# Kernel optimization log

Hardware: AMD Instinct MI355X
Metric: run time of the kernel (lower is better)

The kernel has to match this reference:

```python
import jax, jax.numpy as jnp
import numpy as np


def setup_inputs() -> dict:
    key = jax.random.key(0)
    k1, k2, k3, k4 = jax.random.split(key, 4)
    B, S, E, H = 8, 2048, 1024, 64
    x = jax.random.normal(k1, (B, S, E), dtype=jnp.float32)
    scale = 1.0 / np.sqrt(E)
    Wq = jax.random.normal(k2, (E, H), dtype=jnp.float32) * scale
    Wk = jax.random.normal(k3, (E, H), dtype=jnp.float32) * scale
    Wv = jax.random.normal(k4, (E, H), dtype=jnp.float32) * scale
    return {"x": x, "Wq": Wq, "Wk": Wk, "Wv": Wv}


def reference(x, Wq, Wk, Wv):
    # x: [B, S, E]; Wq/Wk/Wv: [E, H]
    B, S, E = x.shape
    H = Wq.shape[1]
    q = x @ Wq  # [B, S, H]
    k = x @ Wk
    v = x @ Wv
    inv_sqrt_h = 1.0 / jnp.sqrt(jnp.asarray(H, dtype=x.dtype))
    att = jnp.einsum("bqh,bkh->bqk", q, k) * inv_sqrt_h  # [B, S, S]
    causal = jnp.tril(jnp.ones((S, S), dtype=bool))
    att = jnp.where(causal, att, jnp.asarray(-jnp.inf, dtype=att.dtype))
    att = jax.nn.softmax(att, axis=-1)
    # dropout p=0.0 (eval) -> identity
    return jnp.einsum("bqk,bkh->bqh", att, v)  # [B, S, H]
```

## Files before the change

kernel.cpp:

```cpp
#include <hip/hip_runtime.h>
#include <math.h>

typedef __attribute__((ext_vector_type(8))) short bf16x8;
typedef __attribute__((ext_vector_type(16))) float fx16;

#define SEQ 2048
#define HD 64

__device__ __forceinline__ unsigned f2bf_bits(float f){
  unsigned u = __float_as_uint(f);
  return (u + 0x7fffu + ((u >> 16) & 1u)) >> 16;
}
__device__ __forceinline__ unsigned cvt_pk_bf16(float a, float b){
  unsigned r;
  asm("v_cvt_pk_bf16_f32 %0, %1, %2" : "=v"(r) : "v"(a), "v"(b));
  return r;
}
union U8 { bf16x8 v; short s[8]; unsigned u[4]; };

__device__ __forceinline__ fx16 mfma_bf16(bf16x8 a, bf16x8 b, fx16 c){
  return __builtin_amdgcn_mfma_f32_32x32x16_bf16(a, b, c, 0, 0, 0);
}
__device__ __forceinline__ fx16 fzero(){
  fx16 z;
#pragma unroll
  for (int i = 0; i < 16; ++i) z[i] = 0.f;
  return z;
}

__global__ __launch_bounds__(256) void wconv_kernel(
    const float* __restrict__ Wq, const float* __restrict__ Wk, const float* __restrict__ Wv,
    short* __restrict__ wsB)
{
  int gid = blockIdx.x * 4 + (threadIdx.x >> 6);
  int lane = threadIdx.x & 63;
  int l31 = lane & 31, h = lane >> 5;
  int half = gid & 1;
  int rem = gid >> 1;
  int t = rem % 6;
  int stage = rem / 6;
  int n = t * 32 + l31;
  int mat = n >> 6, col = n & 63;
  const float* W = (mat == 0) ? Wq : (mat == 1) ? Wk : Wv;
  int kbase = stage * 16 + h * 8;
  U8 o;
#pragma unroll
  for (int i = 0; i < 8; ++i) {
    float f = W[(size_t)(kbase + i) * 64 + col];
    unsigned hb = f2bf_bits(f);
    if (half == 0) o.s[i] = (short)hb;
    else {
      float hf = __uint_as_float(hb << 16);
      o.s[i] = (short)f2bf_bits(f - hf);
    }
  }
  *(bf16x8*)(wsB + (size_t)gid * 512 + lane * 8) = o.v;
}

__global__ __launch_bounds__(256, 2) void proj_kernel(
    const float* __restrict__ x, const short* __restrict__ wsB,
    short* __restrict__ qh, short* __restrict__ ql,
    short* __restrict__ kh, short* __restrict__ kl,
    short* __restrict__ vth, short* __restrict__ vtl)
{
  __shared__ float Vb[64 * 68];

  const int tid = threadIdx.x;
  const int lane = tid & 63, w = tid >> 6;
  const int l31 = lane & 31, h = lane >> 5;
  const int m = w & 1;
  const int nset = (w >> 1) * 3;
  const int row0 = blockIdx.x * 64;
  const size_t xrow = (size_t)(row0 + m * 32 + l31) * 1024;

  fx16 accP[3], accQ[3];
#pragma unroll
  for (int t = 0; t < 3; ++t) { accP[t] = fzero(); accQ[t] = fzero(); }

  float4 A0[4][2], A1[4][2];
  bf16x8 B0[6], B1[6];

#define LOADA(AB, C1)                                                   \
  {                                                                     \
    _Pragma("unroll")                                                   \
    for (int ks = 0; ks < 4; ++ks) {                                    \
      int k = (C1) * 64 + ks * 16 + h * 8;                              \
      AB[ks][0] = *(const float4*)(x + xrow + k);                       \
      AB[ks][1] = *(const float4*)(x + xrow + k + 4);                   \
    }                                                                   \
  }

#define LOADB(BB, SR)                                                   \
  {                                                                     \
    _Pragma("unroll")                                                   \
    for (int tt = 0; tt < 3; ++tt) {                                    \
      size_t g2 = ((size_t)(SR) * 6 + nset + tt) * 2;                   \
      BB[tt * 2 + 0] = *(const bf16x8*)(wsB + g2 * 512 + lane * 8);     \
      BB[tt * 2 + 1] = *(const bf16x8*)(wsB + (g2 + 1) * 512 + lane * 8);\
    }                                                                   \
  }

#define STEP(AF, BB)                                                    \
  {                                                                     \
    U8 ah, al;                                                          \
    float xf[8];                                                        \
    xf[0] = AF[0].x; xf[1] = AF[0].y; xf[2] = AF[0].z; xf[3] = AF[0].w; \
    xf[4] = AF[1].x; xf[5] = AF[1].y; xf[6] = AF[1].z; xf[7] = AF[1].w; \
    _Pragma("unroll")                                                   \
    for (int i = 0; i < 8; ++i) {                                       \
      unsigned hb = f2bf_bits(xf[i]);                                   \
      ah.s[i] = (short)hb;                                              \
      float hf = __uint_as_float(hb << 16);                             \
      al.s[i] = (short)f2bf_bits(xf[i] - hf);                           \
    }                                                                   \
    _Pragma("unroll")                                                   \
    for (int tt = 0; tt < 3; ++tt) {                                    \
      accP[tt] = mfma_bf16(ah.v, BB[tt * 2 + 0], accP[tt]);             \
      accQ[tt] = mfma_bf16(ah.v, BB[tt * 2 + 1], accQ[tt]);             \
      accQ[tt] = mfma_bf16(al.v, BB[tt * 2 + 0], accQ[tt]);             \
    }                                                                   \
  }

#define CHUNK(C, ACUR, ANEXT)                                           \
  {                                                                     \
    if ((C) < 15) LOADA(ANEXT, (C) + 1);                                \
    STEP(ACUR[0], B0); if ((C) * 4 + 2 < 64) LOADB(B0, (C) * 4 + 2);    \
    STEP(ACUR[1], B1); if ((C) * 4 + 3 < 64) LOADB(B1, (C) * 4 + 3);    \
    STEP(ACUR[2], B0); if ((C) * 4 + 4 < 64) LOADB(B0, (C) * 4 + 4);    \
    STEP(ACUR[3], B1); if ((C) * 4 + 5 < 64) LOADB(B1, (C) * 4 + 5);    \
  }

  LOADA(A0, 0);
  LOADB(B0, 0);
  LOADB(B1, 1);
  for (int c2 = 0; c2 < 8; ++c2) {
    CHUNK(2 * c2 + 0, A0, A1);
    CHUNK(2 * c2 + 1, A1, A0);
  }
#undef CHUNK
#undef STEP
#undef LOADB
#undef LOADA

#pragma unroll
  for (int t = 0; t < 3; ++t) {
    int nt = nset + t;
    int mat = nt >> 1;
    int colb = (nt & 1) * 32 + l31;
    if (mat < 2) {
      short* dh = (mat == 0) ? qh : kh;
      short* dl = (mat == 0) ? ql : kl;
#pragma unroll
      for (int r = 0; r < 16; ++r) {
        float f = accP[t][r] + accQ[t][r];
        int rowg = row0 + m * 32 + (r & 3) + 8 * (r >> 2) + 4 * h;
        unsigned hb = f2bf_bits(f);
        float hf = __uint_as_float(hb << 16);
        unsigned lb = f2bf_bits(f - hf);
        dh[(size_t)rowg * 64 + colb] = (short)hb;
        dl[(size_t)rowg * 64 + colb] = (short)lb;
      }
    } else {
#pragma unroll
      for (int r = 0; r < 16; ++r) {
        float f = accP[t][r] + accQ[t][r];
        int srel = m * 32 + (r & 3) + 8 * (r >> 2) + 4 * h;
        Vb[srel * 68 + (nt - 4) * 32 + l31] = f;
      }
    }
  }
  __syncthreads();
  {
    int d = tid >> 2, sc = (tid & 3) * 16;
    int bb = row0 >> 11, s0 = row0 & 2047;
    U8 hv0, hv1, lv0, lv1;
#pragma unroll
    for (int ss = 0; ss < 16; ++ss) {
      float f = Vb[(sc + ss) * 68 + d];
      unsigned hb = f2bf_bits(f);
      float hf = __uint_as_float(hb << 16);
      unsigned lb = f2bf_bits(f - hf);
      if (ss < 8) { hv0.s[ss] = (short)hb; lv0.s[ss] = (short)lb; }
      else        { hv1.s[ss - 8] = (short)hb; lv1.s[ss - 8] = (short)lb; }
    }
    size_t o = (size_t)(bb * 64 + d) * 2048 + s0 + sc;
    *(bf16x8*)(vth + o) = hv0.v;  *(bf16x8*)(vth + o + 8) = hv1.v;
    *(bf16x8*)(vtl + o) = lv0.v;  *(bf16x8*)(vtl + o + 8) = lv1.v;
  }
}

__global__ __launch_bounds__(256, 2) void attn_kernel(
    const short* __restrict__ qh, const short* __restrict__ ql,
    const short* __restrict__ kh, const short* __restrict__ kl,
    const short* __restrict__ vth, const short* __restrict__ vtl,
    float* __restrict__ segO, float* __restrict__ segL, float* __restrict__ segM)
{
  __shared__ short Kbuf[2][64 * 128];
  __shared__ short Vbuf[2][64 * 128];

  const int bid = blockIdx.x;
  const int b = bid / 40;
  const int j = bid % 40;
  int qt, ch, nch;
  if (j < 4)       { nch = 1; qt = j;               ch = 0; }
  else if (j < 12) { nch = 2; qt = 4 + (j - 4) / 2; ch = (j - 4) % 2; }
  else if (j < 24) { nch = 3; qt = 8 + (j - 12) / 3; ch = (j - 12) % 3; }
  else             { nch = 4; qt = 12 + (j - 24) / 4; ch = (j - 24) % 4; }
  const int S = 2 * qt + 2;
  const int bs = S / nch, rem = S % nch;
  const int nsteps = bs + (ch < rem ? 1 : 0);
  const int kt0 = ch * bs + (ch < rem ? ch : rem);

  const int tid = threadIdx.x;
  const int lane = tid & 63, w = tid >> 6;
  const int l31 = lane & 31, h = lane >> 5;
  const int qabs = qt * 128 + w * 32 + l31;

  bf16x8 qf0[4], qf1[4];
  {
    size_t qrow = ((size_t)b * 2048 + qabs) * 64;
#pragma unroll
    for (int ds = 0; ds < 4; ++ds) {
      qf0[ds] = *(const bf16x8*)(qh + qrow + ds * 16 + 8 * h);
      qf1[ds] = *(const bf16x8*)(ql + qrow + ds * 16 + 8 * h);
    }
  }

  const int slot = tid & 15;
  const int half = slot >> 3;
  const int sb = (slot & 7) << 4;
  const int rbase = tid >> 4;
  const int d0 = (sb ^ ((rbase & 7) << 4)) >> 1;
  const short* ksrc = half ? kl : kh;
  const short* vsrc = half ? vtl : vth;
  const int woff = rbase * 256 + half * 128 + sb;

  fx16 accA0 = fzero(), accA1 = fzero(), accB0 = fzero(), accB1 = fzero();
  float Mrun = -3e38f, lrun = 0.f;
  const int sw = (l31 & 7) << 4;

  bf16x8 kreg[4], vreg[4];
#pragma unroll
  for (int jj = 0; jj < 4; ++jj) {
    kreg[jj] = *(const bf16x8*)(ksrc + ((size_t)b * 2048 + (size_t)kt0 * 64 + rbase + 16 * jj) * 64 + d0);
    vreg[jj] = *(const bf16x8*)(vsrc + ((size_t)(b * 64 + rbase + 16 * jj)) * 2048 + kt0 * 64 + d0);
  }
#pragma unroll
  for (int jj = 0; jj < 4; ++jj) {
    *(bf16x8*)((char*)Kbuf[0] + woff + jj * 4096) = kreg[jj];
    *(bf16x8*)((char*)Vbuf[0] + woff + jj * 4096) = vreg[jj];
  }
  __syncthreads();

  for (int it = 0; it < nsteps; ++it) {
    const int kt = kt0 + it;
    const int p = it & 1;
    const bool hasnext = (it + 1 < nsteps);
    if (hasnext) {
      int kn = kt + 1;
#pragma unroll
      for (int jj = 0; jj < 4; ++jj) {
        kreg[jj] = *(const bf16x8*)(ksrc + ((size_t)b * 2048 + (size_t)kn * 64 + rbase + 16 * jj) * 64 + d0);
        vreg[jj] = *(const bf16x8*)(vsrc + ((size_t)(b * 64 + rbase + 16 * jj)) * 2048 + kn * 64 + d0);
      }
    }

#pragma unroll
    for (int ms = 0; ms < 2; ++ms) {
      fx16 stA = fzero(), stB = fzero(), stC = fzero();
      {
        const char* arow = (const char*)Kbuf[p] + (ms * 32 + l31) * 256;
#pragma unroll
        for (int ds = 0; ds < 4; ++ds) {
          const int kb = ds * 32 + 16 * h;
          bf16x8 ah = *(const bf16x8*)(arow + (kb ^ sw));
          bf16x8 al = *(const bf16x8*)(arow + 128 + (kb ^ sw));
          stA = mfma_bf16(ah, qf0[ds], stA);
          stB = mfma_bf16(ah, qf1[ds], stB);
          stC = mfma_bf16(al, qf0[ds], stC);
        }
      }
      float sv[16];
      const int kbase = kt * 64 + ms * 32;
      const bool diag = (kbase + 31 > qt * 128 + w * 32);
#pragma unroll
      for (int r = 0; r < 16; ++r) {
        float s = (stA[r] + stB[r] + stC[r]) * 0.125f;
        if (diag) {
          int ka = kbase + (r & 3) + 8 * (r >> 2) + 4 * h;
          if (ka > qabs) s = -3e38f;
        }
        sv[r] = s;
      }
      float tm = sv[0];
#pragma unroll
      for (int r = 1; r < 16; ++r) tm = fmaxf(tm, sv[r]);
      tm = fmaxf(tm, __shfl_xor(tm, 32, 64));
      float Mnew = fmaxf(Mrun, tm);
      float alpha = __expf(Mrun - Mnew);
      Mrun = Mnew;
      float pvv[16]; float psum = 0.f;
#pragma unroll
      for (int r = 0; r < 16; ++r) { pvv[r] = __expf(sv[r] - Mnew); psum += pvv[r]; }
      psum += __shfl_xor(psum, 32, 64);
      lrun = lrun * alpha + psum;
#pragma unroll
      for (int r = 0; r < 16; ++r) {
        accA0[r] *= alpha; accA1[r] *= alpha; accB0[r] *= alpha; accB1[r] *= alpha;
      }
      unsigned chv[8], clv[8];
#pragma unroll
      for (int q2 = 0; q2 < 8; ++q2) {
        unsigned c = cvt_pk_bf16(pvv[2 * q2], pvv[2 * q2 + 1]);
        chv[q2] = c;
        float f0 = __uint_as_float(c << 16);
        float f1 = __uint_as_float(c & 0xffff0000u);
        clv[q2] = cvt_pk_bf16(pvv[2 * q2] - f0, pvv[2 * q2 + 1] - f1);
      }
#pragma unroll
      for (int kp = 0; kp < 2; ++kp) {
        U8 ph, pl;
        {
          unsigned c0 = chv[4 * kp], c1 = chv[4 * kp + 1], c2 = chv[4 * kp + 2], c3 = chv[4 * kp + 3];
          unsigned x0 = (unsigned)__shfl_xor((int)c0, 32, 64);
          unsigned x1 = (unsigned)__shfl_xor((int)c1, 32, 64);
          unsigned x2 = (unsigned)__shfl_xor((int)c2, 32, 64);
          unsigned x3 = (unsigned)__shfl_xor((int)c3, 32, 64);
          ph.u[0] = h ? x2 : c0;  ph.u[1] = h ? x3 : c1;
          ph.u[2] = h ? c2 : x0;  ph.u[3] = h ? c3 : x1;
          c0 = clv[4 * kp]; c1 = clv[4 * kp + 1]; c2 = clv[4 * kp + 2]; c3 = clv[4 * kp + 3];
          x0 = (unsigned)__shfl_xor((int)c0, 32, 64);
          x1 = (unsigned)__shfl_xor((int)c1, 32, 64);
          x2 = (unsigned)__shfl_xor((int)c2, 32, 64);
          x3 = (unsigned)__shfl_xor((int)c3, 32, 64);
          pl.u[0] = h ? x2 : c0;  pl.u[1] = h ? x3 : c1;
          pl.u[2] = h ? c2 : x0;  pl.u[3] = h ? c3 : x1;
        }
        const int kbv = ms * 64 + kp * 32 + 16 * h;
#pragma unroll
        for (int md = 0; md < 2; ++md) {
          const char* vrow = (const char*)Vbuf[p] + (md * 32 + l31) * 256;
          bf16x8 vh = *(const bf16x8*)(vrow + (kbv ^ sw));
          bf16x8 vl = *(const bf16x8*)(vrow + 128 + (kbv ^ sw));
          if (md == 0) {
            accA0 = mfma_bf16(vh, ph.v, accA0);
            accB0 = mfma_bf16(vh, pl.v, accB0);
            accB0 = mfma_bf16(vl, ph.v, accB0);
          } else {
            accA1 = mfma_bf16(vh, ph.v, accA1);
            accB1 = mfma_bf16(vh, pl.v, accB1);
            accB1 = mfma_bf16(vl, ph.v, accB1);
          }
        }
      }
    }

    if (hasnext) {
#pragma unroll
      for (int jj = 0; jj < 4; ++jj) {
        *(bf16x8*)((char*)Kbuf[p ^ 1] + woff + jj * 4096) = kreg[jj];
        *(bf16x8*)((char*)Vbuf[p ^ 1] + woff + jj * 4096) = vreg[jj];
      }
    }
    __syncthreads();
  }

  float* o = segO + (size_t)bid * (64 * 128);
#pragma unroll
  for (int md = 0; md < 2; ++md) {
#pragma unroll
    for (int r = 0; r < 16; ++r) {
      int d = md * 32 + (r & 3) + 8 * (r >> 2) + 4 * h;
      float val = md ? (accA1[r] + accB1[r]) : (accA0[r] + accB0[r]);
      o[d * 128 + w * 32 + l31] = val;
    }
  }
  if (h == 0) {
    segL[(size_t)bid * 128 + w * 32 + l31] = lrun;
    segM[(size_t)bid * 128 + w * 32 + l31] = Mrun;
  }
}

__global__ __launch_bounds__(256) void combine_kernel(
    const float* __restrict__ segO, const float* __restrict__ segL,
    const float* __restrict__ segM, float* __restrict__ out)
{
  __shared__ float Sc[4][128];
  __shared__ float Linv[128];
  __shared__ float Ot[64 * 132];

  const int bq = blockIdx.x;
  const int b = bq >> 4, qt = bq & 15;
  const int g = qt >> 2, nch = g + 1;
  const int base = (g == 0) ? qt
                 : (g == 1) ? 4 + (qt - 4) * 2
                 : (g == 2) ? 12 + (qt - 8) * 3
                 : 24 + (qt - 12) * 4;
  const int slot0 = b * 40 + base;
  const int tid = threadIdx.x;

  if (tid < 128) {
    const int q = tid;
    float M = -3e38f;
    for (int c = 0; c < nch; ++c)
      M = fmaxf(M, segM[(size_t)(slot0 + c) * 128 + q]);
    float L = 0.f;
    for (int c = 0; c < nch; ++c) {
      float s = __expf(segM[(size_t)(slot0 + c) * 128 + q] - M);
      Sc[c][q] = s;
      L += s * segL[(size_t)(slot0 + c) * 128 + q];
    }
    Linv[q] = 1.f / L;
  }
  __syncthreads();
  {
    const int dr = tid >> 5;
    const int qc = (tid & 31) * 4;
    for (int dd = dr; dd < 64; dd += 8) {
      float4 acc = {0.f, 0.f, 0.f, 0.f};
      for (int c = 0; c < nch; ++c) {
        float4 v = *(const float4*)(segO + (size_t)(slot0 + c) * 8192 + dd * 128 + qc);
        acc.x += Sc[c][qc + 0] * v.x;
        acc.y += Sc[c][qc + 1] * v.y;
        acc.z += Sc[c][qc + 2] * v.z;
        acc.w += Sc[c][qc + 3] * v.w;
      }
      *(float4*)&Ot[dd * 132 + qc] = acc;
    }
  }
  __syncthreads();
  {
    const int q = tid >> 1, dh = (tid & 1) * 32;
    const float inv = Linv[q];
    float* dst = out + ((size_t)b * 2048 + qt * 128 + q) * 64 + dh;
#pragma unroll
    for (int i = 0; i < 8; ++i) {
      float4 o;
      o.x = Ot[(dh + 4 * i + 0) * 132 + q] * inv;
      o.y = Ot[(dh + 4 * i + 1) * 132 + q] * inv;
      o.z = Ot[(dh + 4 * i + 2) * 132 + q] * inv;
      o.w = Ot[(dh + 4 * i + 3) * 132 + q] * inv;
      *(float4*)(dst + 4 * i) = o;
    }
  }
}

extern "C" void kernel_launch(void* const* d_in, const int* in_sizes, int n_in,
                              void* d_out, int out_size, void* d_ws, size_t ws_size,
                              hipStream_t stream) {
  const float* x  = (const float*)d_in[0];
  const float* Wq = (const float*)d_in[1];
  const float* Wk = (const float*)d_in[2];
  const float* Wv = (const float*)d_in[3];

  char* wsb = (char*)d_ws;
  short* wsB = (short*)(wsb + 0);
  short* qh  = (short*)(wsb + 786432);
  short* ql  = (short*)(wsb + 2883584);
  short* kh  = (short*)(wsb + 4980736);
  short* kl  = (short*)(wsb + 7077888);
  short* vth = (short*)(wsb + 9175040);
  short* vtl = (short*)(wsb + 11272192);
  float* segO = (float*)(wsb + 13369344);
  float* segL = (float*)(wsb + 23855104);
  float* segM = (float*)(wsb + 24018944);

  wconv_kernel<<<192, 256, 0, stream>>>(Wq, Wk, Wv, wsB);
  proj_kernel<<<256, 256, 0, stream>>>(x, wsB, qh, ql, kh, kl, vth, vtl);
  attn_kernel<<<320, 256, 0, stream>>>(qh, ql, kh, kl, vth, vtl, segO, segL, segM);
  combine_kernel<<<128, 256, 0, stream>>>(segO, segL, segM, (float*)d_out);
}
```

Before: 99.05 us.

## Rework attention into single-wave 32-query blocks and stage projection input via LDS

The attention kernel is restructured into 2304 single-wavefront blocks, each owning 32 queries and a split of key tiles. It loads K and V fragments straight from global memory instead of double-buffering them through LDS, and brackets the MFMA sections with s_setprio. The projection kernel now stages x tiles into swizzled LDS with global_load_lds double buffering and uses packed bf16 conversion, and the combine kernel is reindexed for the new segment layout. The aim is more parallelism and fewer barriers, at the cost of K/V reuse across waves (more global/L2 traffic) and a larger segment workspace.

Result: slower. 132.1 us (+33.4%).

```diff
diff --git a/kernel.cpp b/kernel.cpp
--- a/kernel.cpp
+++ b/kernel.cpp
@@ -16,6 +16,8 @@
   asm("v_cvt_pk_bf16_f32 %0, %1, %2" : "=v"(r) : "v"(a), "v"(b));
   return r;
 }
+__device__ __forceinline__ float lo16f(unsigned u){ return __uint_as_float(u << 16); }
+__device__ __forceinline__ float hi16f(unsigned u){ return __uint_as_float(u & 0xffff0000u); }
 union U8 { bf16x8 v; short s[8]; unsigned u[4]; };
 
 __device__ __forceinline__ fx16 mfma_bf16(bf16x8 a, bf16x8 b, fx16 c){
@@ -57,90 +59,82 @@
   *(bf16x8*)(wsB + (size_t)gid * 512 + lane * 8) = o.v;
 }
 
-__global__ __launch_bounds__(256, 2) void proj_kernel(
+__global__ __launch_bounds__(256) void proj_kernel(
     const float* __restrict__ x, const short* __restrict__ wsB,
     short* __restrict__ qh, short* __restrict__ ql,
     short* __restrict__ kh, short* __restrict__ kl,
     short* __restrict__ vth, short* __restrict__ vtl)
 {
+  __shared__ float Xs[2][4096];
   __shared__ float Vb[64 * 68];
 
   const int tid = threadIdx.x;
   const int lane = tid & 63, w = tid >> 6;
   const int l31 = lane & 31, h = lane >> 5;
-  const int m = w & 1;
+  const int mw = w & 1;
   const int nset = (w >> 1) * 3;
   const int row0 = blockIdx.x * 64;
-  const size_t xrow = (size_t)(row0 + m * 32 + l31) * 1024;
+
+  const int stg_row = tid >> 4;
+  const int stg_c = (tid & 15) ^ (stg_row & 7);
+  const size_t stg_off = (size_t)stg_row * 1024 + stg_c * 4;
 
   fx16 accP[3], accQ[3];
 #pragma unroll
   for (int t = 0; t < 3; ++t) { accP[t] = fzero(); accQ[t] = fzero(); }
 
-  float4 A0[4][2], A1[4][2];
-  bf16x8 B0[6], B1[6];
-
-#define LOADA(AB, C1)                                                   \
-  {                                                                     \
-    _Pragma("unroll")                                                   \
-    for (int ks = 0; ks < 4; ++ks) {                                    \
-      int k = (C1) * 64 + ks * 16 + h * 8;                              \
-      AB[ks][0] = *(const float4*)(x + xrow + k);                       \
-      AB[ks][1] = *(const float4*)(x + xrow + k + 4);                   \
-    }                                                                   \
-  }
-
-#define LOADB(BB, SR)                                                   \
-  {                                                                     \
-    _Pragma("unroll")                                                   \
-    for (int tt = 0; tt < 3; ++tt) {                                    \
-      size_t g2 = ((size_t)(SR) * 6 + nset + tt) * 2;                   \
-      BB[tt * 2 + 0] = *(const bf16x8*)(wsB + g2 * 512 + lane * 8);     \
-      BB[tt * 2 + 1] = *(const bf16x8*)(wsB + (g2 + 1) * 512 + lane * 8);\
-    }                                                                   \
-  }
-
-#define STEP(AF, BB)                                                    \
-  {                                                                     \
-    U8 ah, al;                                                          \
-    float xf[8];                                                        \
-    xf[0] = AF[0].x; xf[1] = AF[0].y; xf[2] = AF[0].z; xf[3] = AF[0].w; \
-    xf[4] = AF[1].x; xf[5] = AF[1].y; xf[6] = AF[1].z; xf[7] = AF[1].w; \
-    _Pragma("unroll")                                                   \
-    for (int i = 0; i < 8; ++i) {                                       \
-      unsigned hb = f2bf_bits(xf[i]);                                   \
-      ah.s[i] = (short)hb;                                              \
-      float hf = __uint_as_float(hb << 16);                             \
-      al.s[i] = (short)f2bf_bits(xf[i] - hf);                           \
-    }                                                                   \
-    _Pragma("unroll")                                                   \
-    for (int tt = 0; tt < 3; ++tt) {                                    \
-      accP[tt] = mfma_bf16(ah.v, BB[tt * 2 + 0], accP[tt]);             \
-      accQ[tt] = mfma_bf16(ah.v, BB[tt * 2 + 1], accQ[tt]);             \
-      accQ[tt] = mfma_bf16(al.v, BB[tt * 2 + 0], accQ[tt]);             \
-    }                                                                   \
-  }
-
-#define CHUNK(C, ACUR, ANEXT)                                           \
-  {                                                                     \
-    if ((C) < 15) LOADA(ANEXT, (C) + 1);                                \
-    STEP(ACUR[0], B0); if ((C) * 4 + 2 < 64) LOADB(B0, (C) * 4 + 2);    \
-    STEP(ACUR[1], B1); if ((C) * 4 + 3 < 64) LOADB(B1, (C) * 4 + 3);    \
-    STEP(ACUR[2], B0); if ((C) * 4 + 4 < 64) LOADB(B0, (C) * 4 + 4);    \
-    STEP(ACUR[3], B1); if ((C) * 4 + 5 < 64) LOADB(B1, (C) * 4 + 5);    \
-  }
-
-  LOADA(A0, 0);
-  LOADB(B0, 0);
-  LOADB(B1, 1);
-  for (int c2 = 0; c2 < 8; ++c2) {
-    CHUNK(2 * c2 + 0, A0, A1);
-    CHUNK(2 * c2 + 1, A1, A0);
-  }
-#undef CHUNK
-#undef STEP
-#undef LOADB
-#undef LOADA
+  {
+    const float* gs = x + (size_t)row0 * 1024 + 0 * 64 + stg_off;
+    char* lb = (char*)&Xs[0][0];
+#pragma unroll
+    for (int i = 0; i < 4; ++i)
+      __builtin_amdgcn_global_load_lds(
+        (const __attribute__((address_space(1))) float*)(gs + (size_t)i * 16 * 1024),
+        (__attribute__((address_space(3))) float*)(lb + i * 4096 + tid * 16), 16, 0, 0);
+  }
+  __syncthreads();
+
+  const int arow = mw * 32 + l31;
+  const int rsw = arow & 7;
+
+  for (int step = 0; step < 16; ++step) {
+    const int p = step & 1;
+    if (step < 15) {
+      const float* gs = x + (size_t)row0 * 1024 + (step + 1) * 64 + stg_off;
+      char* lb = (char*)&Xs[p ^ 1][0];
+#pragma unroll
+      for (int i = 0; i < 4; ++i)
+        __builtin_amdgcn_global_load_lds(
+          (const __attribute__((address_space(1))) float*)(gs + (size_t)i * 16 * 1024),
+          (__attribute__((address_space(3))) float*)(lb + i * 4096 + tid * 16), 16, 0, 0);
+    }
+    const char* xb = (const char*)&Xs[p][0] + arow * 256;
+#pragma unroll
+    for (int ks = 0; ks < 4; ++ks) {
+      float4 fa = *(const float4*)(xb + (((ks * 4 + h * 2)     ^ rsw) * 16));
+      float4 fb = *(const float4*)(xb + (((ks * 4 + h * 2 + 1) ^ rsw) * 16));
+      U8 ah, al;
+      ah.u[0] = cvt_pk_bf16(fa.x, fa.y);
+      ah.u[1] = cvt_pk_bf16(fa.z, fa.w);
+      ah.u[2] = cvt_pk_bf16(fb.x, fb.y);
+      ah.u[3] = cvt_pk_bf16(fb.z, fb.w);
+      al.u[0] = cvt_pk_bf16(fa.x - lo16f(ah.u[0]), fa.y - hi16f(ah.u[0]));
+      al.u[1] = cvt_pk_bf16(fa.z - lo16f(ah.u[1]), fa.w - hi16f(ah.u[1]));
+      al.u[2] = cvt_pk_bf16(fb.x - lo16f(ah.u[2]), fb.y - hi16f(ah.u[2]));
+      al.u[3] = cvt_pk_bf16(fb.z - lo16f(ah.u[3]), fb.w - hi16f(ah.u[3]));
+      const int sidx = step * 4 + ks;
+#pragma unroll
+      for (int tt = 0; tt < 3; ++tt) {
+        const size_t g2 = ((size_t)sidx * 6 + nset + tt) * 2;
+        bf16x8 Bh = *(const bf16x8*)(wsB + g2 * 512 + lane * 8);
+        bf16x8 Bl = *(const bf16x8*)(wsB + g2 * 512 + 512 + lane * 8);
+        accP[tt] = mfma_bf16(ah.v, Bh, accP[tt]);
+        accQ[tt] = mfma_bf16(ah.v, Bl, accQ[tt]);
+        accQ[tt] = mfma_bf16(al.v, Bh, accQ[tt]);
+      }
+    }
+    __syncthreads();
+  }
 
 #pragma unroll
   for (int t = 0; t < 3; ++t) {
@@ -153,7 +147,7 @@
 #pragma unroll
       for (int r = 0; r < 16; ++r) {
         float f = accP[t][r] + accQ[t][r];
-        int rowg = row0 + m * 32 + (r & 3) + 8 * (r >> 2) + 4 * h;
+        int rowg = row0 + mw * 32 + (r & 3) + 8 * (r >> 2) + 4 * h;
         unsigned hb = f2bf_bits(f);
         float hf = __uint_as_float(hb << 16);
         unsigned lb = f2bf_bits(f - hf);
@@ -164,7 +158,7 @@
 #pragma unroll
       for (int r = 0; r < 16; ++r) {
         float f = accP[t][r] + accQ[t][r];
-        int srel = m * 32 + (r & 3) + 8 * (r >> 2) + 4 * h;
+        int srel = mw * 32 + (r & 3) + 8 * (r >> 2) + 4 * h;
         Vb[srel * 68 + (nt - 4) * 32 + l31] = f;
       }
     }
@@ -189,32 +183,29 @@
   }
 }
 
-__global__ __launch_bounds__(256, 2) void attn_kernel(
+__global__ __launch_bounds__(64) void attn_kernel(
     const short* __restrict__ qh, const short* __restrict__ ql,
     const short* __restrict__ kh, const short* __restrict__ kl,
     const short* __restrict__ vth, const short* __restrict__ vtl,
     float* __restrict__ segO, float* __restrict__ segL, float* __restrict__ segM)
 {
-  __shared__ short Kbuf[2][64 * 128];
-  __shared__ short Vbuf[2][64 * 128];
-
   const int bid = blockIdx.x;
-  const int b = bid / 40;
-  const int j = bid % 40;
-  int qt, ch, nch;
-  if (j < 4)       { nch = 1; qt = j;               ch = 0; }
-  else if (j < 12) { nch = 2; qt = 4 + (j - 4) / 2; ch = (j - 4) % 2; }
-  else if (j < 24) { nch = 3; qt = 8 + (j - 12) / 3; ch = (j - 12) % 3; }
-  else             { nch = 4; qt = 12 + (j - 24) / 4; ch = (j - 24) % 4; }
-  const int S = 2 * qt + 2;
-  const int bs = S / nch, rem = S % nch;
-  const int nsteps = bs + (ch < rem ? 1 : 0);
-  const int kt0 = ch * bs + (ch < rem ? ch : rem);
-
-  const int tid = threadIdx.x;
-  const int lane = tid & 63, w = tid >> 6;
+  const int b = bid & 7;
+  const int r = bid >> 3;
+  int g = 0;
+  while (r >= 4 * (g + 1) * (g + 2)) ++g;
+  const int rr = r - 4 * g * (g + 1);
+  const int qt = g * 8 + rr / (g + 1);
+  const int sg = rr % (g + 1);
+  const int nk = qt + 1;
+  const int nsg = g + 1;
+  const int bs = nk / nsg, rem = nk % nsg;
+  const int nsteps = bs + (sg < rem ? 1 : 0);
+  const int kt0 = sg * bs + (sg < rem ? sg : rem);
+
+  const int lane = threadIdx.x;
   const int l31 = lane & 31, h = lane >> 5;
-  const int qabs = qt * 128 + w * 32 + l31;
+  const int qabs = qt * 32 + l31;
 
   bf16x8 qf0[4], qf1[4];
   {
@@ -226,158 +217,115 @@
     }
   }
 
-  const int slot = tid & 15;
-  const int half = slot >> 3;
-  const int sb = (slot & 7) << 4;
-  const int rbase = tid >> 4;
-  const int d0 = (sb ^ ((rbase & 7) << 4)) >> 1;
-  const short* ksrc = half ? kl : kh;
-  const short* vsrc = half ? vtl : vth;
-  const int woff = rbase * 256 + half * 128 + sb;
-
   fx16 accA0 = fzero(), accA1 = fzero(), accB0 = fzero(), accB1 = fzero();
   float Mrun = -3e38f, lrun = 0.f;
-  const int sw = (l31 & 7) << 4;
-
-  bf16x8 kreg[4], vreg[4];
-#pragma unroll
-  for (int jj = 0; jj < 4; ++jj) {
-    kreg[jj] = *(const bf16x8*)(ksrc + ((size_t)b * 2048 + (size_t)kt0 * 64 + rbase + 16 * jj) * 64 + d0);
-    vreg[jj] = *(const bf16x8*)(vsrc + ((size_t)(b * 64 + rbase + 16 * jj)) * 2048 + kt0 * 64 + d0);
-  }
-#pragma unroll
-  for (int jj = 0; jj < 4; ++jj) {
-    *(bf16x8*)((char*)Kbuf[0] + woff + jj * 4096) = kreg[jj];
-    *(bf16x8*)((char*)Vbuf[0] + woff + jj * 4096) = vreg[jj];
-  }
-  __syncthreads();
 
   for (int it = 0; it < nsteps; ++it) {
     const int kt = kt0 + it;
-    const int p = it & 1;
-    const bool hasnext = (it + 1 < nsteps);
-    if (hasnext) {
-      int kn = kt + 1;
-#pragma unroll
-      for (int jj = 0; jj < 4; ++jj) {
-        kreg[jj] = *(const bf16x8*)(ksrc + ((size_t)b * 2048 + (size_t)kn * 64 + rbase + 16 * jj) * 64 + d0);
-        vreg[jj] = *(const bf16x8*)(vsrc + ((size_t)(b * 64 + rbase + 16 * jj)) * 2048 + kn * 64 + d0);
-      }
-    }
-
-#pragma unroll
-    for (int ms = 0; ms < 2; ++ms) {
-      fx16 stA = fzero(), stB = fzero(), stC = fzero();
+    const size_t koff = ((size_t)b * 2048 + (size_t)kt * 32 + l31) * 64 + 8 * h;
+    bf16x8 kah[4], kal[4];
+#pragma unroll
+    for (int ds = 0; ds < 4; ++ds) {
+      kah[ds] = *(const bf16x8*)(kh + koff + ds * 16);
+      kal[ds] = *(const bf16x8*)(kl + koff + ds * 16);
+    }
+    fx16 stA = fzero(), stB = fzero();
+    __builtin_amdgcn_s_setprio(1);
+#pragma unroll
+    for (int ds = 0; ds < 4; ++ds) {
+      stA = mfma_bf16(kah[ds], qf0[ds], stA);
+      stB = mfma_bf16(kah[ds], qf1[ds], stB);
+      stB = mfma_bf16(kal[ds], qf0[ds], stB);
+    }
+    __builtin_amdgcn_s_setprio(0);
+
+    bf16x8 vfh[2][2], vfl[2][2];
+#pragma unroll
+    for (int kp = 0; kp < 2; ++kp)
+#pragma unroll
+      for (int md = 0; md < 2; ++md) {
+        const size_t vrow = (size_t)(b * 64 + md * 32 + l31) * 2048 + kt * 32 + kp * 16 + 8 * h;
+        vfh[kp][md] = *(const bf16x8*)(vth + vrow);
+        vfl[kp][md] = *(const bf16x8*)(vtl + vrow);
+      }
+
+    float sv[16];
+    const bool diag = (kt == qt);
+#pragma unroll
+    for (int rr2 = 0; rr2 < 16; ++rr2) {
+      float s = (stA[rr2] + stB[rr2]) * 0.125f;
+      if (diag) {
+        int ka = kt * 32 + (rr2 & 3) + 8 * (rr2 >> 2) + 4 * h;
+        if (ka > qabs) s = -3e38f;
+      }
+      sv[rr2] = s;
+    }
+    float tm = sv[0];
+#pragma unroll
+    for (int rr2 = 1; rr2 < 16; ++rr2) tm = fmaxf(tm, sv[rr2]);
+    tm = fmaxf(tm, __shfl_xor(tm, 32, 64));
+    float Mnew = fmaxf(Mrun, tm);
+    float alpha = __expf(Mrun - Mnew);
+    Mrun = Mnew;
+    float pvv[16]; float psum = 0.f;
+#pragma unroll
+    for (int rr2 = 0; rr2 < 16; ++rr2) { pvv[rr2] = __expf(sv[rr2] - Mnew); psum += pvv[rr2]; }
+    psum += __shfl_xor(psum, 32, 64);
+    lrun = lrun * alpha + psum;
+#pragma unroll
+    for (int rr2 = 0; rr2 < 16; ++rr2) {
+      accA0[rr2] *= alpha; accA1[rr2] *= alpha; accB0[rr2] *= alpha; accB1[rr2] *= alpha;
+    }
+    unsigned chv[8], clv[8];
+#pragma unroll
+    for (int q2 = 0; q2 < 8; ++q2) {
+      unsigned c = cvt_pk_bf16(pvv[2 * q2], pvv[2 * q2 + 1]);
+      chv[q2] = c;
+      clv[q2] = cvt_pk_bf16(pvv[2 * q2] - lo16f(c), pvv[2 * q2 + 1] - hi16f(c));
+    }
+#pragma unroll
+    for (int kp = 0; kp < 2; ++kp) {
+      U8 ph, pl;
       {
-        const char* arow = (const char*)Kbuf[p] + (ms * 32 + l31) * 256;
-#pragma unroll
-        for (int ds = 0; ds < 4; ++ds) {
-          const int kb = ds * 32 + 16 * h;
-          bf16x8 ah = *(const bf16x8*)(arow + (kb ^ sw));
-          bf16x8 al = *(const bf16x8*)(arow + 128 + (kb ^ sw));
-          stA = mfma_bf16(ah, qf0[ds], stA);
-          stB = mfma_bf16(ah, qf1[ds], stB);
-          stC = mfma_bf16(al, qf0[ds], stC);
-        }
-      }
-      float sv[16];
-      const int kbase = kt * 64 + ms * 32;
-      const bool diag = (kbase + 31 > qt * 128 + w * 32);
-#pragma unroll
-      for (int r = 0; r < 16; ++r) {
-        float s = (stA[r] + stB[r] + stC[r]) * 0.125f;
-        if (diag) {
-          int ka = kbase + (r & 3) + 8 * (r >> 2) + 4 * h;
-          if (ka > qabs) s = -3e38f;
-        }
-        sv[r] = s;
-      }
-      float tm = sv[0];
-#pragma unroll
-      for (int r = 1; r < 16; ++r) tm = fmaxf(tm, sv[r]);
-      tm = fmaxf(tm, __shfl_xor(tm, 32, 64));
-      float Mnew = fmaxf(Mrun, tm);
-      float alpha = __expf(Mrun - Mnew);
-      Mrun = Mnew;
-      float pvv[16]; float psum = 0.f;
-#pragma unroll
-      for (int r = 0; r < 16; ++r) { pvv[r] = __expf(sv[r] - Mnew); psum += pvv[r]; }
-      psum += __shfl_xor(psum, 32, 64);
-      lrun = lrun * alpha + psum;
-#pragma unroll
-      for (int r = 0; r < 16; ++r) {
-        accA0[r] *= alpha; accA1[r] *= alpha; accB0[r] *= alpha; accB1[r] *= alpha;
-      }
-      unsigned chv[8], clv[8];
-#pragma unroll
-      for (int q2 = 0; q2 < 8; ++q2) {
-        unsigned c = cvt_pk_bf16(pvv[2 * q2], pvv[2 * q2 + 1]);
-        chv[q2] = c;
-        float f0 = __uint_as_float(c << 16);
-        float f1 = __uint_as_float(c & 0xffff0000u);
-        clv[q2] = cvt_pk_bf16(pvv[2 * q2] - f0, pvv[2 * q2 + 1] - f1);
-      }
-#pragma unroll
-      for (int kp = 0; kp < 2; ++kp) {
-        U8 ph, pl;
-        {
-          unsigned c0 = chv[4 * kp], c1 = chv[4 * kp + 1], c2 = chv[4 * kp + 2], c3 = chv[4 * kp + 3];
-          unsigned x0 = (unsigned)__shfl_xor((int)c0, 32, 64);
-          unsigned x1 = (unsigned)__shfl_xor((int)c1, 32, 64);
-          unsigned x2 = (unsigned)__shfl_xor((int)c2, 32, 64);
-          unsigned x3 = (unsigned)__shfl_xor((int)c3, 32, 64);
-          ph.u[0] = h ? x2 : c0;  ph.u[1] = h ? x3 : c1;
-          ph.u[2] = h ? c2 : x0;  ph.u[3] = h ? c3 : x1;
-          c0 = clv[4 * kp]; c1 = clv[4 * kp + 1]; c2 = clv[4 * kp + 2]; c3 = clv[4 * kp + 3];
-          x0 = (unsigned)__shfl_xor((int)c0, 32, 64);
-          x1 = (unsigned)__shfl_xor((int)c1, 32, 64);
-          x2 = (unsigned)__shfl_xor((int)c2, 32, 64);
-          x3 = (unsigned)__shfl_xor((int)c3, 32, 64);
-          pl.u[0] = h ? x2 : c0;  pl.u[1] = h ? x3 : c1;
-          pl.u[2] = h ? c2 : x0;  pl.u[3] = h ? c3 : x1;
-        }
-        const int kbv = ms * 64 + kp * 32 + 16 * h;
-#pragma unroll
-        for (int md = 0; md < 2; ++md) {
-          const char* vrow = (const char*)Vbuf[p] + (md * 32 + l31) * 256;
-          bf16x8 vh = *(const bf16x8*)(vrow + (kbv ^ sw));
-          bf16x8 vl = *(const bf16x8*)(vrow + 128 + (kbv ^ sw));
-          if (md == 0) {
-            accA0 = mfma_bf16(vh, ph.v, accA0);
-            accB0 = mfma_bf16(vh, pl.v, accB0);
-            accB0 = mfma_bf16(vl, ph.v, accB0);
-          } else {
-            accA1 = mfma_bf16(vh, ph.v, accA1);
-            accB1 = mfma_bf16(vh, pl.v, accB1);
-            accB1 = mfma_bf16(vl, ph.v, accB1);
-          }
-        }
-      }
-    }
-
-    if (hasnext) {
-#pragma unroll
-      for (int jj = 0; jj < 4; ++jj) {
-        *(bf16x8*)((char*)Kbuf[p ^ 1] + woff + jj * 4096) = kreg[jj];
-        *(bf16x8*)((char*)Vbuf[p ^ 1] + woff + jj * 4096) = vreg[jj];
-      }
-    }
-    __syncthreads();
-  }
-
-  float* o = segO + (size_t)bid * (64 * 128);
+        unsigned c0 = chv[4 * kp], c1 = chv[4 * kp + 1], c2 = chv[4 * kp + 2], c3 = chv[4 * kp + 3];
+        unsigned x0 = (unsigned)__shfl_xor((int)c0, 32, 64);
+        unsigned x1 = (unsigned)__shfl_xor((int)c1, 32, 64);
+        unsigned x2 = (unsigned)__shfl_xor((int)c2, 32, 64);
+        unsigned x3 = (unsigned)__shfl_xor((int)c3, 32, 64);
+        ph.u[0] = h ? x2 : c0;  ph.u[1] = h ? x3 : c1;
+        ph.u[2] = h ? c2 : x0;  ph.u[3] = h ? c3 : x1;
+        c0 = clv[4 * kp]; c1 = clv[4 * kp + 1]; c2 = clv[4 * kp + 2]; c3 = clv[4 * kp + 3];
+        x0 = (unsigned)__shfl_xor((int)c0, 32, 64);
+        x1 = (unsigned)__shfl_xor((int)c1, 32, 64);
+        x2 = (unsigned)__shfl_xor((int)c2, 32, 64);
+        x3 = (unsigned)__shfl_xor((int)c3, 32, 64);
+        pl.u[0] = h ? x2 : c0;  pl.u[1] = h ? x3 : c1;
+        pl.u[2] = h ? c2 : x0;  pl.u[3] = h ? c3 : x1;
+      }
+      __builtin_amdgcn_s_setprio(1);
+      accA0 = mfma_bf16(vfh[kp][0], ph.v, accA0);
+      accB0 = mfma_bf16(vfh[kp][0], pl.v, accB0);
+      accB0 = mfma_bf16(vfl[kp][0], ph.v, accB0);
+      accA1 = mfma_bf16(vfh[kp][1], ph.v, accA1);
+      accB1 = mfma_bf16(vfh[kp][1], pl.v, accB1);
+      accB1 = mfma_bf16(vfl[kp][1], ph.v, accB1);
+      __builtin_amdgcn_s_setprio(0);
+    }
+  }
+
+  float* o = segO + (size_t)bid * 2048;
 #pragma unroll
   for (int md = 0; md < 2; ++md) {
 #pragma unroll
-    for (int r = 0; r < 16; ++r) {
-      int d = md * 32 + (r & 3) + 8 * (r >> 2) + 4 * h;
-      float val = md ? (accA1[r] + accB1[r]) : (accA0[r] + accB0[r]);
-      o[d * 128 + w * 32 + l31] = val;
+    for (int rr2 = 0; rr2 < 16; ++rr2) {
+      int d = md * 32 + (rr2 & 3) + 8 * (rr2 >> 2) + 4 * h;
+      float val = md ? (accA1[rr2] + accB1[rr2]) : (accA0[rr2] + accB0[rr2]);
+      o[d * 32 + l31] = val;
     }
   }
   if (h == 0) {
-    segL[(size_t)bid * 128 + w * 32 + l31] = lrun;
-    segM[(size_t)bid * 128 + w * 32 + l31] = Mrun;
+    segL[(size_t)bid * 32 + l31] = lrun;
+    segM[(size_t)bid * 32 + l31] = Mrun;
   }
 }
 
@@ -385,61 +333,56 @@
     const float* __restrict__ segO, const float* __restrict__ segL,
     const float* __restrict__ segM, float* __restrict__ out)
 {
-  __shared__ float Sc[4][128];
-  __shared__ float Linv[128];
-  __shared__ float Ot[64 * 132];
+  __shared__ float Sc[8][32];
+  __shared__ float Linv[32];
+  __shared__ float Ot[64 * 40];
 
   const int bq = blockIdx.x;
-  const int b = bq >> 4, qt = bq & 15;
-  const int g = qt >> 2, nch = g + 1;
-  const int base = (g == 0) ? qt
-                 : (g == 1) ? 4 + (qt - 4) * 2
-                 : (g == 2) ? 12 + (qt - 8) * 3
-                 : 24 + (qt - 12) * 4;
-  const int slot0 = b * 40 + base;
+  const int b = bq >> 6, qt = bq & 63;
+  const int g = qt >> 3, nsg = g + 1;
+  const int base = 4 * g * (g + 1) + (qt & 7) * nsg;
   const int tid = threadIdx.x;
 
-  if (tid < 128) {
-    const int q = tid;
+  if (tid < 32) {
     float M = -3e38f;
-    for (int c = 0; c < nch; ++c)
-      M = fmaxf(M, segM[(size_t)(slot0 + c) * 128 + q]);
+    for (int s = 0; s < nsg; ++s)
+      M = fmaxf(M, segM[(size_t)((base + s) * 8 + b) * 32 + tid]);
     float L = 0.f;
-    for (int c = 0; c < nch; ++c) {
-      float s = __expf(segM[(size_t)(slot0 + c) * 128 + q] - M);
-      Sc[c][q] = s;
-      L += s * segL[(size_t)(slot0 + c) * 128 + q];
-    }
-    Linv[q] = 1.f / L;
+    for (int s = 0; s < nsg; ++s) {
+      float e = __expf(segM[(size_t)((base + s) * 8 + b) * 32 + tid] - M);
+      Sc[s][tid] = e;
+      L += e * segL[(size_t)((base + s) * 8 + b) * 32 + tid];
+    }
+    Linv[tid] = 1.f / L;
   }
   __syncthreads();
   {
-    const int dr = tid >> 5;
-    const int qc = (tid & 31) * 4;
-    for (int dd = dr; dd < 64; dd += 8) {
+#pragma unroll
+    for (int i = tid; i < 512; i += 256) {
+      int d = i >> 3, q4 = (i & 7) * 4;
       float4 acc = {0.f, 0.f, 0.f, 0.f};
-      for (int c = 0; c < nch; ++c) {
-        float4 v = *(const float4*)(segO + (size_t)(slot0 + c) * 8192 + dd * 128 + qc);
-        acc.x += Sc[c][qc + 0] * v.x;
-        acc.y += Sc[c][qc + 1] * v.y;
-        acc.z += Sc[c][qc + 2] * v.z;
-        acc.w += Sc[c][qc + 3] * v.w;
-      }
-      *(float4*)&Ot[dd * 132 + qc] = acc;
+      for (int s = 0; s < nsg; ++s) {
+        float4 v = *(const float4*)(segO + (size_t)((base + s) * 8 + b) * 2048 + d * 32 + q4);
+        acc.x += Sc[s][q4 + 0] * v.x;
+        acc.y += Sc[s][q4 + 1] * v.y;
+        acc.z += Sc[s][q4 + 2] * v.z;
+        acc.w += Sc[s][q4 + 3] * v.w;
+      }
+      *(float4*)&Ot[d * 40 + q4] = acc;
     }
   }
   __syncthreads();
   {
-    const int q = tid >> 1, dh = (tid & 1) * 32;
+    const int q = tid >> 3, dc = (tid & 7) * 8;
     const float inv = Linv[q];
-    float* dst = out + ((size_t)b * 2048 + qt * 128 + q) * 64 + dh;
-#pragma unroll
-    for (int i = 0; i < 8; ++i) {
+    float* dst = out + ((size_t)b * 2048 + qt * 32 + q) * 64 + dc;
+#pragma unroll
+    for (int i = 0; i < 2; ++i) {
       float4 o;
-      o.x = Ot[(dh + 4 * i + 0) * 132 + q] * inv;
-      o.y = Ot[(dh + 4 * i + 1) * 132 + q] * inv;
-      o.z = Ot[(dh + 4 * i + 2) * 132 + q] * inv;
-      o.w = Ot[(dh + 4 * i + 3) * 132 + q] * inv;
+      o.x = Ot[(dc + 4 * i + 0) * 40 + q] * inv;
+      o.y = Ot[(dc + 4 * i + 1) * 40 + q] * inv;
+      o.z = Ot[(dc + 4 * i + 2) * 40 + q] * inv;
+      o.w = Ot[(dc + 4 * i + 3) * 40 + q] * inv;
       *(float4*)(dst + 4 * i) = o;
     }
   }
@@ -462,11 +405,11 @@
   short* vth = (short*)(wsb + 9175040);
   short* vtl = (short*)(wsb + 11272192);
   float* segO = (float*)(wsb + 13369344);
-  float* segL = (float*)(wsb + 23855104);
-  float* segM = (float*)(wsb + 24018944);
+  float* segL = (float*)(wsb + 32243712);
+  float* segM = (float*)(wsb + 32538624);
 
   wconv_kernel<<<192, 256, 0, stream>>>(Wq, Wk, Wv, wsB);
   proj_kernel<<<256, 256, 0, stream>>>(x, wsB, qh, ql, kh, kl, vth, vtl);
-  attn_kernel<<<320, 256, 0, stream>>>(qh, ql, kh, kl, vth, vtl, segO, segL, segM);
-  combine_kernel<<<128, 256, 0, stream>>>(segO, segL, segM, (float*)d_out);
-}
+  attn_kernel<<<2304, 64, 0, stream>>>(qh, ql, kh, kl, vth, vtl, segO, segL, segM);
+  combine_kernel<<<512, 256, 0, stream>>>(segO, segL, segM, (float*)d_out);
+}
```
